# Kernel tuning notes

Measured on AMD Instinct MI355X. Metric: run time of the kernel, lower is better.

Reference implementation:

```python
import jax, jax.numpy as jnp
import numpy as np

S, B, D, H = 2048, 2, 1024, 16
DK = D // H


def setup_inputs() -> dict:
    key = jax.random.key(0)
    k1, k2, k3 = jax.random.split(key, 3)
    x = jax.random.normal(k1, (S, B, D), dtype=jnp.float32)
    # xavier-uniform-like scale for weights
    w_qkv = jax.random.normal(k2, (3 * D, D), dtype=jnp.float32) * (1.0 / np.sqrt(D))
    w_out = jax.random.normal(k3, (D, D), dtype=jnp.float32) * (1.0 / np.sqrt(D))
    b_out = jnp.zeros((D,), dtype=jnp.float32)
    return {"x": x, "w_qkv": w_qkv, "w_out": w_out, "b_out": b_out}


def reference(x, w_qkv, w_out, b_out):
    seq_len, batch, d_model = x.shape
    n_heads = H
    d_k = d_model // n_heads
    # qkv projection: [S,B,3D]
    qkv = jnp.einsum('sbd,ed->sbe', x, w_qkv)
    qkv = qkv.reshape(seq_len, batch, 3, n_heads, d_k)
    qkv = jnp.transpose(qkv, (2, 1, 3, 0, 4))  # [3,B,H,S,dk]
    q, k, v = qkv[0], qkv[1], qkv[2]
    scores = jnp.einsum('bhqd,bhkd->bhqk', q, k) / jnp.sqrt(jnp.asarray(d_k, x.dtype))
    causal = jnp.triu(jnp.ones((seq_len, seq_len), dtype=bool), k=1)
    scores = jnp.where(causal[None, None], jnp.asarray(-jnp.inf, scores.dtype), scores)
    weights = jax.nn.softmax(scores, axis=-1)
    out = jnp.einsum('bhqk,bhkd->bhqd', weights, v)  # [B,H,S,dk]
    out = jnp.transpose(out, (2, 0, 1, 3)).reshape(seq_len, batch, d_model)
    return jnp.einsum('sbd,ed->sbe', out, w_out) + b_out
```

## Files before the change

### kernel.cpp

```cpp
#include <hip/hip_runtime.h>
#include <cstdint>

typedef _Float16 f16;
typedef _Float16 f16x4 __attribute__((ext_vector_type(4)));
typedef _Float16 f16x8 __attribute__((ext_vector_type(8)));
typedef float f32x4 __attribute__((ext_vector_type(4)));

#define MFMA16(a, b, c) __builtin_amdgcn_mfma_f32_16x16x32_f16(a, b, c, 0, 0, 0)
#define QSCALE 0.1803368801111243f

__device__ __forceinline__ void gload_lds16(const void* g, void* l) {
    __builtin_amdgcn_global_load_lds((__attribute__((address_space(1))) void*)(g),
                                     (__attribute__((address_space(3))) void*)(l),
                                     16, 0, 0);
}


__global__ void cast_all(const float* __restrict__ x, const float* __restrict__ wqv,
                         const float* __restrict__ wo, f16* __restrict__ out) {
    int i = blockIdx.x * blockDim.x + threadIdx.x;
    const float* src; int li;
    if (i < 1048576)      { src = x;   li = i; }
    else if (i < 1835008) { src = wqv; li = i - 1048576; }
    else                  { src = wo;  li = i - 1835008; }
    float4 v = reinterpret_cast<const float4*>(src)[li];
    f16x4 o = {(f16)v.x, (f16)v.y, (f16)v.z, (f16)v.w};
    reinterpret_cast<f16x4*>(out)[i] = o;
}

__global__ __launch_bounds__(256, 3) void gemm_qkv(
    const f16* __restrict__ A, const f16* __restrict__ B,
    f16* __restrict__ outq, f16* __restrict__ outk, f16* __restrict__ outvt)
{
    __shared__ f16 As[3][128 * 32];
    __shared__ f16 Bs[3][128 * 32];
    const int tid = threadIdx.x;
    const int lane = tid & 63;
    const int wave = tid >> 6;
    const int wm = wave >> 1, wn = wave & 1;
    const int bm = blockIdx.y * 128, bn = blockIdx.x * 128;
    const int fr = lane & 15, fq = lane >> 4;

    const int srow = tid >> 2;
    const int su = (tid & 3) ^ (srow & 3) ^ ((srow >> 2) & 3);
    const int uoff = (fq ^ (fr & 3) ^ ((fr >> 2) & 3)) * 8;

    f32x4 acc[4][4] = {};

    auto stg = [&](int tt, int buf) {
        const int k0 = tt * 32;
        gload_lds16(&A[(bm + srow) * 1024 + k0 + su * 8],      &As[buf][tid * 8]);
        gload_lds16(&A[(bm + 64 + srow) * 1024 + k0 + su * 8], &As[buf][2048 + tid * 8]);
        gload_lds16(&B[(bn + srow) * 1024 + k0 + su * 8],      &Bs[buf][tid * 8]);
        gload_lds16(&B[(bn + 64 + srow) * 1024 + k0 + su * 8], &Bs[buf][2048 + tid * 8]);
    };

    auto step = [&](int t, int buf) {
        const int b2 = (buf + 2 >= 3) ? (buf - 1) : (buf + 2);
        if (t < 30) stg(t + 2, b2);
        f16x8 af[4], bf[4];
#pragma unroll
        for (int mt = 0; mt < 4; ++mt)
            af[mt] = *(const f16x8*)&As[buf][(wm * 64 + mt * 16 + fr) * 32 + uoff];
#pragma unroll
        for (int nt = 0; nt < 4; ++nt)
            bf[nt] = *(const f16x8*)&Bs[buf][(wn * 64 + nt * 16 + fr) * 32 + uoff];
        __builtin_amdgcn_s_setprio(1);
#pragma unroll
        for (int mt = 0; mt < 4; ++mt)
#pragma unroll
            for (int nt = 0; nt < 4; ++nt)
                acc[mt][nt] = MFMA16(af[mt], bf[nt], acc[mt][nt]);
        __builtin_amdgcn_s_setprio(0);
        if (t < 30) { asm volatile("s_waitcnt vmcnt(4)" ::: "memory"); }
        else        { asm volatile("s_waitcnt vmcnt(0)" ::: "memory"); }
        __builtin_amdgcn_s_barrier();
        __builtin_amdgcn_sched_barrier(0);
    };

    stg(0, 0);
    stg(1, 1);
    asm volatile("s_waitcnt vmcnt(4)" ::: "memory");
    __builtin_amdgcn_s_barrier();
    __builtin_amdgcn_sched_barrier(0);
#pragma unroll 1
    for (int tb = 0; tb < 30; tb += 3) {
        step(tb, 0);
        step(tb + 1, 1);
        step(tb + 2, 2);
    }
    step(30, 0);
    step(31, 1);

    const int x = blockIdx.x;
    if (x < 16) {
        f16* base = (x < 8) ? outq : outk;
        const float scale = (x < 8) ? QSCALE : 1.0f;
        const int coloff = (x < 8) ? bn : (bn - 1024);
#pragma unroll
        for (int mt = 0; mt < 4; ++mt)
#pragma unroll
            for (int nt = 0; nt < 4; ++nt)
#pragma unroll
                for (int i = 0; i < 4; ++i) {
                    int row = bm + wm * 64 + mt * 16 + fq * 4 + i;
                    int col = coloff + wn * 64 + nt * 16 + fr;
                    int s = row >> 1, b = row & 1;
                    int h = col >> 6, dk = col & 63;
                    base[((b * 16 + h) * 2048 + s) * 64 + dk] = (f16)(acc[mt][nt][i] * scale);
                }
    } else {
        const int xb = x - 16;
        const int s0 = bm >> 1;
        f16* Ts = &As[0][0];
#pragma unroll
        for (int p = 0; p < 2; ++p) {
            __syncthreads();
            if (wn == p) {
#pragma unroll
                for (int mt = 0; mt < 4; ++mt)
#pragma unroll
                    for (int nt = 0; nt < 4; ++nt)
#pragma unroll
                        for (int i = 0; i < 4; ++i) {
                            int row = wm * 64 + mt * 16 + fq * 4 + i;
                            int cl = nt * 16 + fr;
                            Ts[(cl * 2 + (row & 1)) * 76 + (row >> 1)] = (f16)acc[mt][nt][i];
                        }
            }
            __syncthreads();
            const int h = xb * 2 + p;
            const int sj = tid & 7;
#pragma unroll
            for (int it = 0; it < 4; ++it) {
                int idx = (tid >> 3) + it * 32;
                int bsel = idx & 1, dk = idx >> 1;
                f16x8 v = *(const f16x8*)&Ts[(dk * 2 + bsel) * 76 + sj * 8];
                *(f16x8*)&outvt[((bsel * 16 + h) * 64 + dk) * 2048 + s0 + sj * 8] = v;
            }
        }
    }
}

__global__ __launch_bounds__(512) void attn_kernel(
    const f16* __restrict__ qg, const f16* __restrict__ kg,
    const f16* __restrict__ vtg, f16* __restrict__ attn)
{
    __shared__ f16 Ks[2][64 * 64];
    __shared__ f16 Vs[2][64 * 64];
    __shared__ f16 plds[8][16 * 72];
    const int tid = threadIdx.x;
    const int lane = tid & 63;
    const int wave = tid >> 6;
    const int qpair = blockIdx.x;
    const int bh = blockIdx.y;
    const int b = bh >> 4, h = bh & 15;
    const int fr = lane & 15, fq = lane >> 4;

    const bool isB = wave < 4;
    const int w4 = wave & 3;
    const int qrow = (isB ? (31 - qpair) : qpair) * 64 + w4 * 16;
    const int nB = 32 - qpair;
    const int nK = isB ? nB : (qpair + 1);

    const f16* Q  = qg  + bh * 2048 * 64;
    const f16* K  = kg  + bh * 2048 * 64;
    const f16* VT = vtg + bh * 64 * 2048;
    f16* P = plds[wave];

    const int sr = tid >> 3;
    const int scu = (tid & 7) ^ (sr & 7);

    f16x8 aq0 = *(const f16x8*)&Q[(qrow + fr) * 64 + fq * 8];
    f16x8 aq1 = *(const f16x8*)&Q[(qrow + fr) * 64 + 32 + fq * 8];

    f32x4 o[4] = {};
    float l[4] = {};

    auto stage = [&](int kc, int buf) {
        const int kb = kc * 64;
        gload_lds16(&K[(kb + sr) * 64 + scu * 8], &Ks[buf][tid * 8]);
        gload_lds16(&VT[sr * 2048 + kb + scu * 8], &Vs[buf][tid * 8]);
    };

    auto compute = [&](int kb, const f16* Ksb, const f16* Vsb, bool domask) {
        f32x4 sc[4] = {};
#pragma unroll
        for (int ct = 0; ct < 4; ++ct) {
            int r = ct * 16 + fr;
            f16x8 b0 = *(const f16x8*)&Ksb[r * 64 + ((fq ^ (r & 7)) * 8)];
            f16x8 b1 = *(const f16x8*)&Ksb[r * 64 + (((4 + fq) ^ (r & 7)) * 8)];
            sc[ct] = MFMA16(aq0, b0, sc[ct]);
            sc[ct] = MFMA16(aq1, b1, sc[ct]);
        }
        if (domask) {
#pragma unroll
            for (int ct = 0; ct < 4; ++ct) {
                int kcol = kb + ct * 16 + fr;
#pragma unroll
                for (int i = 0; i < 4; ++i)
                    if (kcol > qrow + fq * 4 + i) sc[ct][i] = -1e30f;
            }
        }
#pragma unroll
        for (int i = 0; i < 4; ++i) {
            float p0 = __builtin_amdgcn_exp2f(sc[0][i]);
            float p1 = __builtin_amdgcn_exp2f(sc[1][i]);
            float p2 = __builtin_amdgcn_exp2f(sc[2][i]);
            float p3 = __builtin_amdgcn_exp2f(sc[3][i]);
            l[i] += (p0 + p1) + (p2 + p3);
            P[(fq * 4 + i) * 72 + fr]      = (f16)p0;
            P[(fq * 4 + i) * 72 + 16 + fr] = (f16)p1;
            P[(fq * 4 + i) * 72 + 32 + fr] = (f16)p2;
            P[(fq * 4 + i) * 72 + 48 + fr] = (f16)p3;
        }
        f16x8 ap0 = *(const f16x8*)&P[fr * 72 + fq * 8];
        f16x8 ap1 = *(const f16x8*)&P[fr * 72 + 32 + fq * 8];
#pragma unroll
        for (int nt = 0; nt < 4; ++nt) {
            int dk = nt * 16 + fr;
            f16x8 bv0 = *(const f16x8*)&Vsb[dk * 64 + ((fq ^ (dk & 7)) * 8)];
            f16x8 bv1 = *(const f16x8*)&Vsb[dk * 64 + (((4 + fq) ^ (dk & 7)) * 8)];
            o[nt] = MFMA16(ap0, bv0, o[nt]);
            o[nt] = MFMA16(ap1, bv1, o[nt]);
        }
    };

    stage(0, 0);
    for (int kc = 0; kc < nB; ++kc) {
        const int kb = kc * 64;
        const int cur = kc & 1;
        __syncthreads();
        if (kc + 1 < nB) stage(kc + 1, cur ^ 1);
        if (kc < nK) compute(kb, Ks[cur], Vs[cur], kb + 63 > qrow);
    }

#pragma unroll
    for (int i = 0; i < 4; ++i) {
        float rs = l[i];
        rs += __shfl_xor(rs, 1);
        rs += __shfl_xor(rs, 2);
        rs += __shfl_xor(rs, 4);
        rs += __shfl_xor(rs, 8);
        float inv = __builtin_amdgcn_rcpf(rs);
        int srow = qrow + fq * 4 + i;
#pragma unroll
        for (int nt = 0; nt < 4; ++nt)
            attn[(srow * 2 + b) * 1024 + h * 64 + nt * 16 + fr] = (f16)(o[nt][i] * inv);
    }
}

__global__ __launch_bounds__(256) void gemm_out(
    const f16* __restrict__ A, const f16* __restrict__ B,
    const float* __restrict__ bias, float* __restrict__ out)
{
    __shared__ f16 As[3][128 * 32];
    __shared__ f16 Bs[3][64 * 32];
    const int tid = threadIdx.x;
    const int lane = tid & 63;
    const int wave = tid >> 6;
    const int wm = wave >> 1, wn = wave & 1;
    const int bm = blockIdx.y * 128, bn = blockIdx.x * 64;
    const int fr = lane & 15, fq = lane >> 4;

    const int srow = tid >> 2;
    const int su = (tid & 3) ^ (srow & 3) ^ ((srow >> 2) & 3);
    const int uoff = (fq ^ (fr & 3) ^ ((fr >> 2) & 3)) * 8;

    f32x4 acc[4][2] = {};

    auto stg = [&](int tt, int buf) {
        const int k0 = tt * 32;
        gload_lds16(&A[(bm + srow) * 1024 + k0 + su * 8],      &As[buf][tid * 8]);
        gload_lds16(&A[(bm + 64 + srow) * 1024 + k0 + su * 8], &As[buf][2048 + tid * 8]);
        gload_lds16(&B[(bn + srow) * 1024 + k0 + su * 8],      &Bs[buf][tid * 8]);
    };

    auto step = [&](int t, int buf) {
        const int b2 = (buf + 2 >= 3) ? (buf - 1) : (buf + 2);
        if (t < 30) stg(t + 2, b2);
        f16x8 af[4], bf[2];
#pragma unroll
        for (int mt = 0; mt < 4; ++mt)
            af[mt] = *(const f16x8*)&As[buf][(wm * 64 + mt * 16 + fr) * 32 + uoff];
#pragma unroll
        for (int nt = 0; nt < 2; ++nt)
            bf[nt] = *(const f16x8*)&Bs[buf][(wn * 32 + nt * 16 + fr) * 32 + uoff];
        __builtin_amdgcn_s_setprio(1);
#pragma unroll
        for (int mt = 0; mt < 4; ++mt)
#pragma unroll
            for (int nt = 0; nt < 2; ++nt)
                acc[mt][nt] = MFMA16(af[mt], bf[nt], acc[mt][nt]);
        __builtin_amdgcn_s_setprio(0);
        if (t < 30) { asm volatile("s_waitcnt vmcnt(3)" ::: "memory"); }
        else        { asm volatile("s_waitcnt vmcnt(0)" ::: "memory"); }
        __builtin_amdgcn_s_barrier();
        __builtin_amdgcn_sched_barrier(0);
    };

    stg(0, 0);
    stg(1, 1);
    asm volatile("s_waitcnt vmcnt(3)" ::: "memory");
    __builtin_amdgcn_s_barrier();
    __builtin_amdgcn_sched_barrier(0);
#pragma unroll 1
    for (int tb = 0; tb < 30; tb += 3) {
        step(tb, 0);
        step(tb + 1, 1);
        step(tb + 2, 2);
    }
    step(30, 0);
    step(31, 1);

#pragma unroll
    for (int mt = 0; mt < 4; ++mt)
#pragma unroll
        for (int nt = 0; nt < 2; ++nt)
#pragma unroll
            for (int i = 0; i < 4; ++i) {
                int row = bm + wm * 64 + mt * 16 + fq * 4 + i;
                int col = bn + wn * 32 + nt * 16 + fr;
                out[row * 1024 + col] = acc[mt][nt][i] + bias[col];
            }
}

extern "C" void kernel_launch(void* const* d_in, const int* in_sizes, int n_in,
                              void* d_out, int out_size, void* d_ws, size_t ws_size,
                              hipStream_t stream)
{
    const float* x     = (const float*)d_in[0];
    const float* w_qkv = (const float*)d_in[1];
    const float* w_out = (const float*)d_in[2];
    const float* b_out = (const float*)d_in[3];
    float* out = (float*)d_out;

    char* ws = (char*)d_ws;
    f16* xh  = (f16*)(ws);
    f16* wqh = (f16*)(ws + 8388608);
    f16* woh = (f16*)(ws + 14680064);
    f16* qh  = (f16*)(ws + 16777216);
    f16* kh  = (f16*)(ws + 25165824);
    f16* vt  = (f16*)(ws + 33554432);
    f16* ah  = (f16*)(ws + 41943040);

    cast_all<<<8192, 256, 0, stream>>>(x, w_qkv, w_out, xh);
    gemm_qkv<<<dim3(24, 32), 256, 0, stream>>>(xh, wqh, qh, kh, vt);
    attn_kernel<<<dim3(16, 32), 512, 0, stream>>>(qh, kh, vt, ah);
    gemm_out<<<dim3(16, 32), 256, 0, stream>>>(ah, woh, b_out, out);
}
```

Before: 176.7 us.

## Give each attention wave 32 query rows and halve block size

The attention kernel now uses 4 waves of 256 threads, each handling 32 query rows (two 16-row MFMA tiles), instead of 8 waves with 16 rows each. Every K/V fragment read from LDS therefore feeds twice as many MFMAs, and each thread issues two staging loads per matrix. The score MFMA operands are swapped so P is written as packed f16x4 and row sums are reduced across quads with a final lane shuffle. This cuts LDS traffic per FLOP and raises ILP, at the cost of more registers per wave and fewer waves per block to hide latency.

```diff
diff --git a/kernel.cpp b/kernel.cpp
--- a/kernel.cpp
+++ b/kernel.cpp
@@ -142,13 +142,13 @@
     }
 }
 
-__global__ __launch_bounds__(512) void attn_kernel(
+__global__ __launch_bounds__(256, 2) void attn_kernel(
     const f16* __restrict__ qg, const f16* __restrict__ kg,
     const f16* __restrict__ vtg, f16* __restrict__ attn)
 {
     __shared__ f16 Ks[2][64 * 64];
     __shared__ f16 Vs[2][64 * 64];
-    __shared__ f16 plds[8][16 * 72];
+    __shared__ f16 plds[4][32 * 72];
     const int tid = threadIdx.x;
     const int lane = tid & 63;
     const int wave = tid >> 6;
@@ -157,72 +157,92 @@
     const int b = bh >> 4, h = bh & 15;
     const int fr = lane & 15, fq = lane >> 4;
 
-    const bool isB = wave < 4;
-    const int w4 = wave & 3;
-    const int qrow = (isB ? (31 - qpair) : qpair) * 64 + w4 * 16;
+    const bool isB = wave < 2;
+    const int w2 = wave & 1;
+    const int qrow = (isB ? (31 - qpair) : qpair) * 64 + w2 * 32;
     const int nB = 32 - qpair;
-    const int nK = isB ? nB : (qpair + 1);
+    const int nK = (qrow >> 6) + 1;
 
     const f16* Q  = qg  + bh * 2048 * 64;
     const f16* K  = kg  + bh * 2048 * 64;
     const f16* VT = vtg + bh * 64 * 2048;
     f16* P = plds[wave];
 
-    const int sr = tid >> 3;
-    const int scu = (tid & 7) ^ (sr & 7);
-
-    f16x8 aq0 = *(const f16x8*)&Q[(qrow + fr) * 64 + fq * 8];
-    f16x8 aq1 = *(const f16x8*)&Q[(qrow + fr) * 64 + 32 + fq * 8];
-
-    f32x4 o[4] = {};
-    float l[4] = {};
+    const int srow = tid >> 3;
+    const int su8 = (tid & 7) ^ (srow & 7);
+
+    f16x8 aq00 = *(const f16x8*)&Q[(qrow + fr) * 64 + fq * 8];
+    f16x8 aq01 = *(const f16x8*)&Q[(qrow + fr) * 64 + 32 + fq * 8];
+    f16x8 aq10 = *(const f16x8*)&Q[(qrow + 16 + fr) * 64 + fq * 8];
+    f16x8 aq11 = *(const f16x8*)&Q[(qrow + 16 + fr) * 64 + 32 + fq * 8];
+
+    f32x4 o[2][4] = {};
+    float lsum[2] = {0.f, 0.f};
 
     auto stage = [&](int kc, int buf) {
         const int kb = kc * 64;
-        gload_lds16(&K[(kb + sr) * 64 + scu * 8], &Ks[buf][tid * 8]);
-        gload_lds16(&VT[sr * 2048 + kb + scu * 8], &Vs[buf][tid * 8]);
+        gload_lds16(&K[(kb + srow) * 64 + su8 * 8],         &Ks[buf][tid * 8]);
+        gload_lds16(&K[(kb + srow + 32) * 64 + su8 * 8],    &Ks[buf][2048 + tid * 8]);
+        gload_lds16(&VT[srow * 2048 + kb + su8 * 8],        &Vs[buf][tid * 8]);
+        gload_lds16(&VT[(srow + 32) * 2048 + kb + su8 * 8], &Vs[buf][2048 + tid * 8]);
     };
 
     auto compute = [&](int kb, const f16* Ksb, const f16* Vsb, bool domask) {
-        f32x4 sc[4] = {};
+        f32x4 sc0[4] = {}, sc1[4] = {};
 #pragma unroll
         for (int ct = 0; ct < 4; ++ct) {
             int r = ct * 16 + fr;
-            f16x8 b0 = *(const f16x8*)&Ksb[r * 64 + ((fq ^ (r & 7)) * 8)];
-            f16x8 b1 = *(const f16x8*)&Ksb[r * 64 + (((4 + fq) ^ (r & 7)) * 8)];
-            sc[ct] = MFMA16(aq0, b0, sc[ct]);
-            sc[ct] = MFMA16(aq1, b1, sc[ct]);
+            f16x8 kf0 = *(const f16x8*)&Ksb[r * 64 + ((fq ^ (r & 7)) * 8)];
+            f16x8 kf1 = *(const f16x8*)&Ksb[r * 64 + (((4 + fq) ^ (r & 7)) * 8)];
+            sc0[ct] = MFMA16(kf0, aq00, sc0[ct]);
+            sc0[ct] = MFMA16(kf1, aq01, sc0[ct]);
+            sc1[ct] = MFMA16(kf0, aq10, sc1[ct]);
+            sc1[ct] = MFMA16(kf1, aq11, sc1[ct]);
         }
         if (domask) {
 #pragma unroll
             for (int ct = 0; ct < 4; ++ct) {
-                int kcol = kb + ct * 16 + fr;
-#pragma unroll
-                for (int i = 0; i < 4; ++i)
-                    if (kcol > qrow + fq * 4 + i) sc[ct][i] = -1e30f;
+                int kk = kb + ct * 16 + fq * 4;
+#pragma unroll
+                for (int i = 0; i < 4; ++i) {
+                    if (kk + i > qrow + fr)      sc0[ct][i] = -1e30f;
+                    if (kk + i > qrow + 16 + fr) sc1[ct][i] = -1e30f;
+                }
             }
         }
-#pragma unroll
-        for (int i = 0; i < 4; ++i) {
-            float p0 = __builtin_amdgcn_exp2f(sc[0][i]);
-            float p1 = __builtin_amdgcn_exp2f(sc[1][i]);
-            float p2 = __builtin_amdgcn_exp2f(sc[2][i]);
-            float p3 = __builtin_amdgcn_exp2f(sc[3][i]);
-            l[i] += (p0 + p1) + (p2 + p3);
-            P[(fq * 4 + i) * 72 + fr]      = (f16)p0;
-            P[(fq * 4 + i) * 72 + 16 + fr] = (f16)p1;
-            P[(fq * 4 + i) * 72 + 32 + fr] = (f16)p2;
-            P[(fq * 4 + i) * 72 + 48 + fr] = (f16)p3;
-        }
-        f16x8 ap0 = *(const f16x8*)&P[fr * 72 + fq * 8];
-        f16x8 ap1 = *(const f16x8*)&P[fr * 72 + 32 + fq * 8];
+        float l0 = 0.f, l1 = 0.f;
+#pragma unroll
+        for (int ct = 0; ct < 4; ++ct) {
+            float p0 = __builtin_amdgcn_exp2f(sc0[ct][0]);
+            float p1 = __builtin_amdgcn_exp2f(sc0[ct][1]);
+            float p2 = __builtin_amdgcn_exp2f(sc0[ct][2]);
+            float p3 = __builtin_amdgcn_exp2f(sc0[ct][3]);
+            l0 += (p0 + p1) + (p2 + p3);
+            f16x4 pk0 = {(f16)p0, (f16)p1, (f16)p2, (f16)p3};
+            *(f16x4*)&P[fr * 72 + ct * 16 + fq * 4] = pk0;
+            float q0 = __builtin_amdgcn_exp2f(sc1[ct][0]);
+            float q1 = __builtin_amdgcn_exp2f(sc1[ct][1]);
+            float q2 = __builtin_amdgcn_exp2f(sc1[ct][2]);
+            float q3 = __builtin_amdgcn_exp2f(sc1[ct][3]);
+            l1 += (q0 + q1) + (q2 + q3);
+            f16x4 pk1 = {(f16)q0, (f16)q1, (f16)q2, (f16)q3};
+            *(f16x4*)&P[(16 + fr) * 72 + ct * 16 + fq * 4] = pk1;
+        }
+        lsum[0] += l0;
+        lsum[1] += l1;
+        f16x8 ap00 = *(const f16x8*)&P[fr * 72 + fq * 8];
+        f16x8 ap01 = *(const f16x8*)&P[fr * 72 + 32 + fq * 8];
+        f16x8 ap10 = *(const f16x8*)&P[(16 + fr) * 72 + fq * 8];
+        f16x8 ap11 = *(const f16x8*)&P[(16 + fr) * 72 + 32 + fq * 8];
 #pragma unroll
         for (int nt = 0; nt < 4; ++nt) {
             int dk = nt * 16 + fr;
             f16x8 bv0 = *(const f16x8*)&Vsb[dk * 64 + ((fq ^ (dk & 7)) * 8)];
             f16x8 bv1 = *(const f16x8*)&Vsb[dk * 64 + (((4 + fq) ^ (dk & 7)) * 8)];
-            o[nt] = MFMA16(ap0, bv0, o[nt]);
-            o[nt] = MFMA16(ap1, bv1, o[nt]);
+            o[0][nt] = MFMA16(ap00, bv0, o[0][nt]);
+            o[0][nt] = MFMA16(ap01, bv1, o[0][nt]);
+            o[1][nt] = MFMA16(ap10, bv0, o[1][nt]);
+            o[1][nt] = MFMA16(ap11, bv1, o[1][nt]);
         }
     };
 
@@ -236,17 +256,20 @@
     }
 
 #pragma unroll
-    for (int i = 0; i < 4; ++i) {
-        float rs = l[i];
-        rs += __shfl_xor(rs, 1);
-        rs += __shfl_xor(rs, 2);
-        rs += __shfl_xor(rs, 4);
-        rs += __shfl_xor(rs, 8);
+    for (int qb = 0; qb < 2; ++qb) {
+        float rs = lsum[qb];
+        rs += __shfl_xor(rs, 16);
+        rs += __shfl_xor(rs, 32);
         float inv = __builtin_amdgcn_rcpf(rs);
-        int srow = qrow + fq * 4 + i;
-#pragma unroll
-        for (int nt = 0; nt < 4; ++nt)
-            attn[(srow * 2 + b) * 1024 + h * 64 + nt * 16 + fr] = (f16)(o[nt][i] * inv);
+#pragma unroll
+        for (int i = 0; i < 4; ++i) {
+            float invi = __shfl(inv, fq * 4 + i);
+            int srow = qrow + qb * 16 + fq * 4 + i;
+#pragma unroll
+            for (int nt = 0; nt < 4; ++nt)
+                attn[(srow * 2 + b) * 1024 + h * 64 + nt * 16 + fr] =
+                    (f16)(o[qb][nt][i] * invi);
+        }
     }
 }
 
@@ -346,6 +369,6 @@
 
     cast_all<<<8192, 256, 0, stream>>>(x, w_qkv, w_out, xh);
     gemm_qkv<<<dim3(24, 32), 256, 0, stream>>>(xh, wqh, qh, kh, vt);
-    attn_kernel<<<dim3(16, 32), 512, 0, stream>>>(qh, kh, vt, ah);
+    attn_kernel<<<dim3(16, 32), 256, 0, stream>>>(qh, kh, vt, ah);
     gemm_out<<<dim3(16, 32), 256, 0, stream>>>(ah, woh, b_out, out);
 }
```

After: 182.1 us. +3.0%, slower.

## Compute transposed scores, pass P via lane shuffles, triple-buffer K/V loads

Applied to the files above, without the earlier changes.

The attention kernel now computes S^T by swapping the MFMA operands, so each lane holds four consecutive key columns for one query row. The P operand for the PV MFMA is then assembled with cross-lane shuffles instead of a round trip through LDS, which removes the per-wave P buffer. K/V staging moves from double to triple buffering with explicit vmcnt waits and raw barriers so loads run two tiles ahead, and MFMA sections are wrapped in s_setprio. The added launch-bounds occupancy hint and extra LDS buffers may raise register or LDS pressure, and the row-sum reduction is reorganised around the new layout.

```diff
diff --git a/kernel.cpp b/kernel.cpp
--- a/kernel.cpp
+++ b/kernel.cpp
@@ -2,6 +2,7 @@
 #include <cstdint>
 
 typedef _Float16 f16;
+typedef _Float16 f16x2 __attribute__((ext_vector_type(2)));
 typedef _Float16 f16x4 __attribute__((ext_vector_type(4)));
 typedef _Float16 f16x8 __attribute__((ext_vector_type(8)));
 typedef float f32x4 __attribute__((ext_vector_type(4)));
@@ -142,13 +143,12 @@
     }
 }
 
-__global__ __launch_bounds__(512) void attn_kernel(
+__global__ __launch_bounds__(512, 6) void attn_kernel(
     const f16* __restrict__ qg, const f16* __restrict__ kg,
     const f16* __restrict__ vtg, f16* __restrict__ attn)
 {
-    __shared__ f16 Ks[2][64 * 64];
-    __shared__ f16 Vs[2][64 * 64];
-    __shared__ f16 plds[8][16 * 72];
+    __shared__ f16 Ks[3][64 * 64];
+    __shared__ f16 Vs[3][64 * 64];
     const int tid = threadIdx.x;
     const int lane = tid & 63;
     const int wave = tid >> 6;
@@ -161,12 +161,11 @@
     const int w4 = wave & 3;
     const int qrow = (isB ? (31 - qpair) : qpair) * 64 + w4 * 16;
     const int nB = 32 - qpair;
-    const int nK = isB ? nB : (qpair + 1);
+    const int nK = (qrow >> 6) + 1;
 
     const f16* Q  = qg  + bh * 2048 * 64;
     const f16* K  = kg  + bh * 2048 * 64;
     const f16* VT = vtg + bh * 64 * 2048;
-    f16* P = plds[wave];
 
     const int sr = tid >> 3;
     const int scu = (tid & 7) ^ (sr & 7);
@@ -175,78 +174,108 @@
     f16x8 aq1 = *(const f16x8*)&Q[(qrow + fr) * 64 + 32 + fq * 8];
 
     f32x4 o[4] = {};
-    float l[4] = {};
-
-    auto stage = [&](int kc, int buf) {
+    float lsum = 0.f;
+
+    const int la = fr + ((fq & 1) << 5);
+    const int lb = la + 16;
+    const bool hi = (fq & 2) != 0;
+
+    auto stage = [&](int kc, f16* Ksb, f16* Vsb) {
         const int kb = kc * 64;
-        gload_lds16(&K[(kb + sr) * 64 + scu * 8], &Ks[buf][tid * 8]);
-        gload_lds16(&VT[sr * 2048 + kb + scu * 8], &Vs[buf][tid * 8]);
+        gload_lds16(&K[(kb + sr) * 64 + scu * 8], &Ksb[tid * 8]);
+        gload_lds16(&VT[sr * 2048 + kb + scu * 8], &Vsb[tid * 8]);
     };
 
     auto compute = [&](int kb, const f16* Ksb, const f16* Vsb, bool domask) {
         f32x4 sc[4] = {};
+        __builtin_amdgcn_s_setprio(1);
 #pragma unroll
         for (int ct = 0; ct < 4; ++ct) {
             int r = ct * 16 + fr;
-            f16x8 b0 = *(const f16x8*)&Ksb[r * 64 + ((fq ^ (r & 7)) * 8)];
-            f16x8 b1 = *(const f16x8*)&Ksb[r * 64 + (((4 + fq) ^ (r & 7)) * 8)];
-            sc[ct] = MFMA16(aq0, b0, sc[ct]);
-            sc[ct] = MFMA16(aq1, b1, sc[ct]);
-        }
+            f16x8 kf0 = *(const f16x8*)&Ksb[r * 64 + ((fq ^ (r & 7)) * 8)];
+            f16x8 kf1 = *(const f16x8*)&Ksb[r * 64 + (((4 + fq) ^ (r & 7)) * 8)];
+            sc[ct] = MFMA16(kf0, aq0, sc[ct]);
+            sc[ct] = MFMA16(kf1, aq1, sc[ct]);
+        }
+        __builtin_amdgcn_s_setprio(0);
         if (domask) {
 #pragma unroll
             for (int ct = 0; ct < 4; ++ct) {
-                int kcol = kb + ct * 16 + fr;
+                int kk = kb + ct * 16 + fq * 4;
 #pragma unroll
                 for (int i = 0; i < 4; ++i)
-                    if (kcol > qrow + fq * 4 + i) sc[ct][i] = -1e30f;
+                    if (kk + i > qrow + fr) sc[ct][i] = -1e30f;
             }
         }
-#pragma unroll
-        for (int i = 0; i < 4; ++i) {
-            float p0 = __builtin_amdgcn_exp2f(sc[0][i]);
-            float p1 = __builtin_amdgcn_exp2f(sc[1][i]);
-            float p2 = __builtin_amdgcn_exp2f(sc[2][i]);
-            float p3 = __builtin_amdgcn_exp2f(sc[3][i]);
-            l[i] += (p0 + p1) + (p2 + p3);
-            P[(fq * 4 + i) * 72 + fr]      = (f16)p0;
-            P[(fq * 4 + i) * 72 + 16 + fr] = (f16)p1;
-            P[(fq * 4 + i) * 72 + 32 + fr] = (f16)p2;
-            P[(fq * 4 + i) * 72 + 48 + fr] = (f16)p3;
-        }
-        f16x8 ap0 = *(const f16x8*)&P[fr * 72 + fq * 8];
-        f16x8 ap1 = *(const f16x8*)&P[fr * 72 + 32 + fq * 8];
+        unsigned P2[4][2];
+#pragma unroll
+        for (int ct = 0; ct < 4; ++ct) {
+            float p0 = __builtin_amdgcn_exp2f(sc[ct][0]);
+            float p1 = __builtin_amdgcn_exp2f(sc[ct][1]);
+            float p2 = __builtin_amdgcn_exp2f(sc[ct][2]);
+            float p3 = __builtin_amdgcn_exp2f(sc[ct][3]);
+            lsum += (p0 + p1) + (p2 + p3);
+            f16x2 e0 = {(f16)p0, (f16)p1};
+            f16x2 e1 = {(f16)p2, (f16)p3};
+            P2[ct][0] = __builtin_bit_cast(unsigned, e0);
+            P2[ct][1] = __builtin_bit_cast(unsigned, e1);
+        }
+        unsigned a0 = __shfl((int)P2[0][0], la), b0 = __shfl((int)P2[1][0], la);
+        unsigned a1 = __shfl((int)P2[0][1], la), b1 = __shfl((int)P2[1][1], la);
+        unsigned a2 = __shfl((int)P2[0][0], lb), b2 = __shfl((int)P2[1][0], lb);
+        unsigned a3 = __shfl((int)P2[0][1], lb), b3 = __shfl((int)P2[1][1], lb);
+        uint4 W0 = {hi ? b0 : a0, hi ? b1 : a1, hi ? b2 : a2, hi ? b3 : a3};
+        f16x8 apk0 = __builtin_bit_cast(f16x8, W0);
+        unsigned c0 = __shfl((int)P2[2][0], la), d0 = __shfl((int)P2[3][0], la);
+        unsigned c1 = __shfl((int)P2[2][1], la), d1 = __shfl((int)P2[3][1], la);
+        unsigned c2 = __shfl((int)P2[2][0], lb), d2 = __shfl((int)P2[3][0], lb);
+        unsigned c3 = __shfl((int)P2[2][1], lb), d3 = __shfl((int)P2[3][1], lb);
+        uint4 W1 = {hi ? d0 : c0, hi ? d1 : c1, hi ? d2 : c2, hi ? d3 : c3};
+        f16x8 apk1 = __builtin_bit_cast(f16x8, W1);
+        __builtin_amdgcn_s_setprio(1);
 #pragma unroll
         for (int nt = 0; nt < 4; ++nt) {
             int dk = nt * 16 + fr;
             f16x8 bv0 = *(const f16x8*)&Vsb[dk * 64 + ((fq ^ (dk & 7)) * 8)];
             f16x8 bv1 = *(const f16x8*)&Vsb[dk * 64 + (((4 + fq) ^ (dk & 7)) * 8)];
-            o[nt] = MFMA16(ap0, bv0, o[nt]);
-            o[nt] = MFMA16(ap1, bv1, o[nt]);
-        }
-    };
-
-    stage(0, 0);
+            o[nt] = MFMA16(apk0, bv0, o[nt]);
+            o[nt] = MFMA16(apk1, bv1, o[nt]);
+        }
+        __builtin_amdgcn_s_setprio(0);
+    };
+
+    stage(0, Ks[0], Vs[0]);
+    stage(1, Ks[1], Vs[1]);
+    asm volatile("s_waitcnt vmcnt(2)" ::: "memory");
+    __builtin_amdgcn_s_barrier();
+    __builtin_amdgcn_sched_barrier(0);
+
+    int cur = 0;
+#pragma unroll 1
     for (int kc = 0; kc < nB; ++kc) {
-        const int kb = kc * 64;
-        const int cur = kc & 1;
-        __syncthreads();
-        if (kc + 1 < nB) stage(kc + 1, cur ^ 1);
-        if (kc < nK) compute(kb, Ks[cur], Vs[cur], kb + 63 > qrow);
-    }
-
+        if (kc + 2 < nB) {
+            int b2 = cur + 2; if (b2 >= 3) b2 -= 3;
+            stage(kc + 2, Ks[b2], Vs[b2]);
+        }
+        if (kc < nK) compute(kc * 64, Ks[cur], Vs[cur], kc * 64 + 63 > qrow);
+        if (kc + 2 < nB) { asm volatile("s_waitcnt vmcnt(2)" ::: "memory"); }
+        else             { asm volatile("s_waitcnt vmcnt(0)" ::: "memory"); }
+        __builtin_amdgcn_s_barrier();
+        __builtin_amdgcn_sched_barrier(0);
+        if (++cur == 3) cur = 0;
+    }
+
+    float rs = lsum;
+    rs += __shfl_xor(rs, 16);
+    rs += __shfl_xor(rs, 32);
+    float inv = __builtin_amdgcn_rcpf(rs);
 #pragma unroll
     for (int i = 0; i < 4; ++i) {
-        float rs = l[i];
-        rs += __shfl_xor(rs, 1);
-        rs += __shfl_xor(rs, 2);
-        rs += __shfl_xor(rs, 4);
-        rs += __shfl_xor(rs, 8);
-        float inv = __builtin_amdgcn_rcpf(rs);
+        float invi = __shfl(inv, fq * 4 + i);
         int srow = qrow + fq * 4 + i;
 #pragma unroll
         for (int nt = 0; nt < 4; ++nt)
-            attn[(srow * 2 + b) * 1024 + h * 64 + nt * 16 + fr] = (f16)(o[nt][i] * inv);
+            attn[(srow * 2 + b) * 1024 + h * 64 + nt * 16 + fr] = (f16)(o[nt][i] * invi);
     }
 }
 
```

New measurement: 177.9 us. Within noise of the previous version (+0.7%).
